# Optimization experiments

Hardware: AMD Instinct MI355X
Metric: run time of the kernel (lower is better)

Reference implementation:

```python
import jax, jax.numpy as jnp
import numpy as np

DIM = 2048
N_HEADS = 16
HEAD_DIM = DIM // N_HEADS
MAX_SEQ_LEN = 2048
THRESHOLD = 0.7
LN_EPS = 1e-5


def _layernorm(x, g, b):
    mu = jnp.mean(x, axis=-1, keepdims=True)
    var = jnp.mean(jnp.square(x - mu), axis=-1, keepdims=True)
    return (x - mu) * jax.lax.rsqrt(var + LN_EPS) * g + b


def _act_quant(x):
    # 8-bit absmax activation quantization (per-tensor), straight-through
    s = 127.0 / jnp.maximum(jnp.max(jnp.abs(x)), 1e-5)
    xq = jnp.clip(jnp.round(x * s), -128.0, 127.0) / s
    return x + jax.lax.stop_gradient(xq - x)


def _ternary_quant(w):
    # W1.58 ternary: zero weights below threshold*mean|w|, scale = mean |w| over survivors
    delta = THRESHOLD * jnp.mean(jnp.abs(w))
    mask = (jnp.abs(w) > delta).astype(w.dtype)
    alpha = jnp.sum(jnp.abs(w) * mask) / jnp.maximum(jnp.sum(mask), 1.0)
    wq = jnp.sign(w) * mask * alpha
    return w + jax.lax.stop_gradient(wq - w)


def _bitlinear(x, w, g, b):
    x = _layernorm(x, g, b)
    xq = _act_quant(x)
    wq = _ternary_quant(w)
    return xq @ wq.T


def _rope_tables():
    inv = 1.0 / (10000.0 ** (np.arange(0, HEAD_DIM, 2, dtype=np.float32) / HEAD_DIM))
    t = np.arange(MAX_SEQ_LEN, dtype=np.float32)
    ang = np.outer(t, inv)  # (max_seq, head_dim/2)
    return jnp.asarray(np.cos(ang)), jnp.asarray(np.sin(ang))


def _apply_rope(x, cos_t, sin_t):
    # Faithful to source: x is (B, H, S, D) and freqs are indexed by x.shape[1] == H
    n = x.shape[1]
    xr = x.reshape(*x.shape[:-1], HEAD_DIM // 2, 2)
    a, b = xr[..., 0], xr[..., 1]
    c = cos_t[:n][None, :, None, :]  # (1, H, 1, D/2)
    s = sin_t[:n][None, :, None, :]
    out = jnp.stack([a * c - b * s, a * s + b * c], axis=-1)
    return out.reshape(x.shape)


def setup_inputs() -> dict:
    key = jax.random.key(0)
    ks = jax.random.split(key, 5)
    std = np.sqrt(2.0 / DIM)
    d = {"x": jax.random.normal(ks[0], (2, MAX_SEQ_LEN, DIM), dtype=jnp.float32)}
    for i, nm in enumerate(["q", "k", "v", "o"]):
        d[f"w_{nm}"] = jax.random.normal(ks[i + 1], (DIM, DIM), dtype=jnp.float32) * std
        d[f"g_{nm}"] = jnp.ones((DIM,), dtype=jnp.float32)
        d[f"b_{nm}"] = jnp.zeros((DIM,), dtype=jnp.float32)
    return d


def reference(x, w_q, g_q, b_q, w_k, g_k, b_k, w_v, g_v, b_v, w_o, g_o, b_o):
    B, S, _ = x.shape
    cos_t, sin_t = _rope_tables()
    scale = HEAD_DIM ** -0.5

    def split_heads(t):
        return t.reshape(B, S, N_HEADS, HEAD_DIM).transpose(0, 2, 1, 3)

    q = split_heads(_bitlinear(x, w_q, g_q, b_q))
    k = split_heads(_bitlinear(x, w_k, g_k, b_k))
    v = split_heads(_bitlinear(x, w_v, g_v, b_v))
    q = _apply_rope(q, cos_t, sin_t)
    k = _apply_rope(k, cos_t, sin_t)
    scores = jnp.einsum("bhsd,bhtd->bhst", q, k) * scale
    attn = jax.nn.softmax(scores, axis=-1)
    out = jnp.einsum("bhst,bhtd->bhsd", attn, v)
    out = out.transpose(0, 2, 1, 3).reshape(B, S, DIM)
    return _bitlinear(out, w_o, g_o, b_o)
```

## Files before the change

### kernel.cpp

```cpp
#include <hip/hip_runtime.h>
#include <math.h>

#define DIM 2048
#define NROWS 4096
#define WN (DIM*DIM)
#define HEADS 16
#define HDIM 128
#define SEQ 2048

typedef __attribute__((ext_vector_type(8))) short short8;
typedef __attribute__((ext_vector_type(8))) _Float16 half8;
typedef __attribute__((ext_vector_type(4))) float floatx4;
typedef __attribute__((ext_vector_type(4))) int intx4;

__device__ __forceinline__ unsigned short f2h(float f) {
  _Float16 h = (_Float16)f;
  return __builtin_bit_cast(unsigned short, h);
}
__device__ __forceinline__ float h2f(unsigned short u) {
  _Float16 h = __builtin_bit_cast(_Float16, u);
  return (float)h;
}
__device__ __forceinline__ unsigned pkh2(float a, float b) {
  return __builtin_bit_cast(unsigned, __builtin_amdgcn_cvt_pkrtz(a, b));
}

__device__ __forceinline__ void gload_lds16(const void* g, void* l) {
  __builtin_amdgcn_global_load_lds(
      (const __attribute__((address_space(1))) unsigned int*)g,
      (__attribute__((address_space(3))) unsigned int*)l, 16, 0, 0);
}

__device__ __forceinline__ float wredSum(float v) {
  #pragma unroll
  for (int o = 1; o < 64; o <<= 1) v += __shfl_xor(v, o);
  return v;
}
__device__ __forceinline__ float wredMax(float v) {
  #pragma unroll
  for (int o = 1; o < 64; o <<= 1) v = fmaxf(v, __shfl_xor(v, o));
  return v;
}

__device__ __forceinline__ float blockReduceSum(float v, float* red) {
  int tid = threadIdx.x;
  red[tid] = v; __syncthreads();
  for (int s = 128; s > 0; s >>= 1) {
    if (tid < s) red[tid] += red[tid + s];
    __syncthreads();
  }
  float r = red[0]; __syncthreads();
  return r;
}

__device__ __forceinline__ const float* pick_w(const float* a, const float* b,
                                               const float* c, const float* d, int i) {
  return i == 0 ? a : i == 1 ? b : i == 2 ? c : d;
}

__global__ __launch_bounds__(256) void w_abs_partial(
    const float* w0, const float* w1, const float* w2, const float* w3, float* part)
{
  const float4* w4 = (const float4*)pick_w(w0, w1, w2, w3, blockIdx.y);
  float s = 0.f;
  for (int i = blockIdx.x * 256 + threadIdx.x; i < WN / 4; i += 1024 * 256) {
    float4 v = w4[i];
    s += fabsf(v.x) + fabsf(v.y) + fabsf(v.z) + fabsf(v.w);
  }
  __shared__ float red[256];
  float t = blockReduceSum(s, red);
  if (threadIdx.x == 0) part[blockIdx.y * 1024 + blockIdx.x] = t;
}

__global__ __launch_bounds__(256) void w_delta_final(const float* part, float* stats)
{
  float s = 0.f;
  for (int i = threadIdx.x; i < 1024; i += 256) s += part[blockIdx.x * 1024 + i];
  __shared__ float red[256];
  float t = blockReduceSum(s, red);
  if (threadIdx.x == 0) stats[blockIdx.x] = 0.7f * (t / (float)WN);
}

__device__ __forceinline__ signed char tq(float v, float delta) {
  if (fabsf(v) > delta) return (v > 0.f) ? (signed char)1 : (signed char)-1;
  return (signed char)0;
}

__global__ __launch_bounds__(256) void w_maskquant(
    const float* w0, const float* w1, const float* w2, const float* w3,
    const float* stats, float* part2, signed char* tern)
{
  int wi = blockIdx.y;
  const float4* w4 = (const float4*)pick_w(w0, w1, w2, w3, wi);
  float delta = stats[wi];
  char4* out = (char4*)(tern + (size_t)wi * WN);
  float s = 0.f, cnt = 0.f;
  for (int i = blockIdx.x * 256 + threadIdx.x; i < WN / 4; i += 1024 * 256) {
    float4 v = w4[i];
    char4 o;
    float a;
    a = fabsf(v.x); if (a > delta) { s += a; cnt += 1.f; } o.x = tq(v.x, delta);
    a = fabsf(v.y); if (a > delta) { s += a; cnt += 1.f; } o.y = tq(v.y, delta);
    a = fabsf(v.z); if (a > delta) { s += a; cnt += 1.f; } o.z = tq(v.z, delta);
    a = fabsf(v.w); if (a > delta) { s += a; cnt += 1.f; } o.w = tq(v.w, delta);
    out[i] = o;
  }
  __shared__ float red[256];
  float ts = blockReduceSum(s, red);
  float tc = blockReduceSum(cnt, red);
  if (threadIdx.x == 0) {
    part2[((size_t)blockIdx.y * 1024 + blockIdx.x) * 2]     = ts;
    part2[((size_t)blockIdx.y * 1024 + blockIdx.x) * 2 + 1] = tc;
  }
}

__global__ __launch_bounds__(256) void w_alpha_final(const float* part2, float* stats)
{
  float s = 0.f, c = 0.f;
  for (int i = threadIdx.x; i < 1024; i += 256) {
    s += part2[((size_t)blockIdx.x * 1024 + i) * 2];
    c += part2[((size_t)blockIdx.x * 1024 + i) * 2 + 1];
  }
  __shared__ float red[256];
  float ts = blockReduceSum(s, red);
  float tc = blockReduceSum(c, red);
  if (threadIdx.x == 0) stats[4 + blockIdx.x] = ts / fmaxf(tc, 1.f);
}

__global__ __launch_bounds__(256) void ln_absmax3(
    const float* __restrict__ x,
    const float* __restrict__ g0, const float* __restrict__ b0,
    const float* __restrict__ g1, const float* __restrict__ b1,
    const float* __restrict__ g2, const float* __restrict__ b2,
    float* __restrict__ pmax)
{
  const int lane = threadIdx.x & 63;
  const int row = blockIdx.x * 4 + (threadIdx.x >> 6);
  const float* xr = x + (size_t)row * DIM;
  float4 a[8];
  float s = 0.f, sq = 0.f;
  #pragma unroll
  for (int j = 0; j < 8; ++j) {
    a[j] = *(const float4*)(xr + j * 256 + lane * 4);
    s  += a[j].x + a[j].y + a[j].z + a[j].w;
    sq += a[j].x*a[j].x + a[j].y*a[j].y + a[j].z*a[j].z + a[j].w*a[j].w;
  }
  s = wredSum(s); sq = wredSum(sq);
  float mu = s * (1.f / DIM);
  float var = sq * (1.f / DIM) - mu * mu;
  float rstd = 1.f / sqrtf(var + 1e-5f);
  const float* gs[3] = {g0, g1, g2};
  const float* bs[3] = {b0, b1, b2};
  #pragma unroll
  for (int p = 0; p < 3; ++p) {
    float m = 0.f;
    #pragma unroll
    for (int j = 0; j < 8; ++j) {
      float4 gg = *(const float4*)(gs[p] + j * 256 + lane * 4);
      float4 bb = *(const float4*)(bs[p] + j * 256 + lane * 4);
      m = fmaxf(m, fabsf((a[j].x - mu) * rstd * gg.x + bb.x));
      m = fmaxf(m, fabsf((a[j].y - mu) * rstd * gg.y + bb.y));
      m = fmaxf(m, fabsf((a[j].z - mu) * rstd * gg.z + bb.z));
      m = fmaxf(m, fabsf((a[j].w - mu) * rstd * gg.w + bb.w));
    }
    m = wredMax(m);
    if (lane == 0) pmax[(size_t)p * NROWS + row] = m;
  }
}

__global__ __launch_bounds__(256) void absmax_final(
    const float* __restrict__ pmax, unsigned* __restrict__ ambits)
{
  const float* src = pmax + (size_t)blockIdx.x * NROWS;
  float m = 0.f;
  for (int i = threadIdx.x; i < NROWS; i += 256) m = fmaxf(m, src[i]);
  m = wredMax(m);
  __shared__ float red[4];
  if ((threadIdx.x & 63) == 0) red[threadIdx.x >> 6] = m;
  __syncthreads();
  if (threadIdx.x == 0)
    ambits[blockIdx.x] = __float_as_uint(fmaxf(fmaxf(red[0], red[1]), fmaxf(red[2], red[3])));
}

__global__ __launch_bounds__(256) void ln_quant3(
    const float* __restrict__ x,
    const float* __restrict__ g0, const float* __restrict__ b0,
    const float* __restrict__ g1, const float* __restrict__ b1,
    const float* __restrict__ g2, const float* __restrict__ b2,
    const unsigned* __restrict__ ambits,
    signed char* __restrict__ xq0, signed char* __restrict__ xq1,
    signed char* __restrict__ xq2)
{
  const int lane = threadIdx.x & 63;
  const int row = blockIdx.x * 4 + (threadIdx.x >> 6);
  const float* xr = x + (size_t)row * DIM;
  float4 a[8];
  float s = 0.f, sq = 0.f;
  #pragma unroll
  for (int j = 0; j < 8; ++j) {
    a[j] = *(const float4*)(xr + j * 256 + lane * 4);
    s  += a[j].x + a[j].y + a[j].z + a[j].w;
    sq += a[j].x*a[j].x + a[j].y*a[j].y + a[j].z*a[j].z + a[j].w*a[j].w;
  }
  s = wredSum(s); sq = wredSum(sq);
  float mu = s * (1.f / DIM);
  float var = sq * (1.f / DIM) - mu * mu;
  float rstd = 1.f / sqrtf(var + 1e-5f);
  const float* gs[3] = {g0, g1, g2};
  const float* bs[3] = {b0, b1, b2};
  signed char* outs[3] = {xq0, xq1, xq2};
  #pragma unroll
  for (int p = 0; p < 3; ++p) {
    float sc = 127.f / fmaxf(__uint_as_float(ambits[p]), 1e-5f);
    #pragma unroll
    for (int j = 0; j < 8; ++j) {
      float4 gg = *(const float4*)(gs[p] + j * 256 + lane * 4);
      float4 bb = *(const float4*)(bs[p] + j * 256 + lane * 4);
      float y0 = (a[j].x - mu) * rstd * gg.x + bb.x;
      float y1 = (a[j].y - mu) * rstd * gg.y + bb.y;
      float y2 = (a[j].z - mu) * rstd * gg.z + bb.z;
      float y3 = (a[j].w - mu) * rstd * gg.w + bb.w;
      char4 q;
      q.x = (signed char)(int)fminf(fmaxf(rintf(y0 * sc), -128.f), 127.f);
      q.y = (signed char)(int)fminf(fmaxf(rintf(y1 * sc), -128.f), 127.f);
      q.z = (signed char)(int)fminf(fmaxf(rintf(y2 * sc), -128.f), 127.f);
      q.w = (signed char)(int)fminf(fmaxf(rintf(y3 * sc), -128.f), 127.f);
      *(char4*)(outs[p] + (size_t)row * DIM + j * 256 + lane * 4) = q;
    }
  }
}

template<int MODE>
__global__ __launch_bounds__(256) void ln_kernel(
    const float* __restrict__ x, const float* __restrict__ g, const float* __restrict__ bias,
    const unsigned* __restrict__ ambits, float* __restrict__ pmax,
    signed char* __restrict__ xq)
{
  const int lane = threadIdx.x & 63;
  const int row = blockIdx.x * 4 + (threadIdx.x >> 6);
  const float* xr = x + (size_t)row * DIM;
  float4 a[8];
  float s = 0.f, sq = 0.f;
  #pragma unroll
  for (int j = 0; j < 8; ++j) {
    a[j] = *(const float4*)(xr + j * 256 + lane * 4);
    s  += a[j].x + a[j].y + a[j].z + a[j].w;
    sq += a[j].x*a[j].x + a[j].y*a[j].y + a[j].z*a[j].z + a[j].w*a[j].w;
  }
  s = wredSum(s); sq = wredSum(sq);
  float mu = s * (1.f / DIM);
  float var = sq * (1.f / DIM) - mu * mu;
  float rstd = 1.f / sqrtf(var + 1e-5f);
  if (MODE == 0) {
    float m = 0.f;
    #pragma unroll
    for (int j = 0; j < 8; ++j) {
      float4 gg = *(const float4*)(g + j * 256 + lane * 4);
      float4 bb = *(const float4*)(bias + j * 256 + lane * 4);
      m = fmaxf(m, fabsf((a[j].x - mu) * rstd * gg.x + bb.x));
      m = fmaxf(m, fabsf((a[j].y - mu) * rstd * gg.y + bb.y));
      m = fmaxf(m, fabsf((a[j].z - mu) * rstd * gg.z + bb.z));
      m = fmaxf(m, fabsf((a[j].w - mu) * rstd * gg.w + bb.w));
    }
    m = wredMax(m);
    if (lane == 0) pmax[row] = m;
  } else {
    float sc = 127.f / fmaxf(__uint_as_float(*ambits), 1e-5f);
    #pragma unroll
    for (int j = 0; j < 8; ++j) {
      float4 gg = *(const float4*)(g + j * 256 + lane * 4);
      float4 bb = *(const float4*)(bias + j * 256 + lane * 4);
      float y0 = (a[j].x - mu) * rstd * gg.x + bb.x;
      float y1 = (a[j].y - mu) * rstd * gg.y + bb.y;
      float y2 = (a[j].z - mu) * rstd * gg.z + bb.z;
      float y3 = (a[j].w - mu) * rstd * gg.w + bb.w;
      char4 q;
      q.x = (signed char)(int)fminf(fmaxf(rintf(y0 * sc), -128.f), 127.f);
      q.y = (signed char)(int)fminf(fmaxf(rintf(y1 * sc), -128.f), 127.f);
      q.z = (signed char)(int)fminf(fmaxf(rintf(y2 * sc), -128.f), 127.f);
      q.w = (signed char)(int)fminf(fmaxf(rintf(y3 * sc), -128.f), 127.f);
      *(char4*)(xq + (size_t)row * DIM + j * 256 + lane * 4) = q;
    }
  }
}

__global__ __launch_bounds__(256) void gemm_qkv(
    const signed char* __restrict__ A0, const signed char* __restrict__ A1,
    const signed char* __restrict__ A2, const signed char* __restrict__ Bt0,
    unsigned short* __restrict__ C0, unsigned short* __restrict__ C1,
    unsigned short* __restrict__ C2t, const float* __restrict__ stats)
{
  const int tid = threadIdx.x;
  const int lane = tid & 63;
  const int w = tid >> 6;
  const int wm = w >> 1, wn = w & 1;
  const int quad = lane >> 4, l16 = lane & 15;
  const int bm = blockIdx.x * 128, bn = blockIdx.y * 128;
  const int z = blockIdx.z;

  const signed char* A  = z == 0 ? A0 : z == 1 ? A1 : A2;
  const signed char* Bt = Bt0 + (size_t)z * WN;

  __shared__ __align__(16) signed char smem[2 * 128 * 128];
  signed char* As = smem;
  signed char* Bs = smem + 128 * 128;

  const int srow_off = lane >> 3;
  const int scol     = (lane & 7) * 16;

  intx4 acc[4][4];
  #pragma unroll
  for (int i = 0; i < 4; ++i)
    #pragma unroll
    for (int j = 0; j < 4; ++j) acc[i][j] = {0, 0, 0, 0};

  for (int k0 = 0; k0 < DIM; k0 += 128) {
    #pragma unroll
    for (int i = 0; i < 4; ++i) {
      int c = i * 4 + w;
      int row = c * 8 + srow_off;
      gload_lds16(A  + (size_t)(bm + row) * DIM + k0 + scol, &As[c * 1024]);
      gload_lds16(Bt + (size_t)(bn + row) * DIM + k0 + scol, &Bs[c * 1024]);
    }
    __syncthreads();
    #pragma unroll
    for (int kc = 0; kc < 2; ++kc) {
      intx4 af[4], bf[4];
      #pragma unroll
      for (int i = 0; i < 4; ++i)
        af[i] = *(const intx4*)&As[(wm * 64 + i * 16 + l16) * 128 + kc * 64 + quad * 16];
      #pragma unroll
      for (int j = 0; j < 4; ++j)
        bf[j] = *(const intx4*)&Bs[(wn * 64 + j * 16 + l16) * 128 + kc * 64 + quad * 16];
      #pragma unroll
      for (int i = 0; i < 4; ++i)
        #pragma unroll
        for (int j = 0; j < 4; ++j)
          acc[i][j] = __builtin_amdgcn_mfma_i32_16x16x64_i8(af[i], bf[j], acc[i][j], 0, 0, 0);
    }
    __syncthreads();
  }

  const unsigned* am = (const unsigned*)(stats + 8);
  float scale = stats[4 + z] * fmaxf(__uint_as_float(am[z]), 1e-5f) * (1.f / 127.f);

  if (z < 2) {
    unsigned short* Cp = z == 0 ? C0 : C1;
    #pragma unroll
    for (int i = 0; i < 4; ++i)
      #pragma unroll
      for (int j = 0; j < 4; ++j)
        #pragma unroll
        for (int r = 0; r < 4; ++r) {
          int m = bm + wm * 64 + i * 16 + quad * 4 + r;
          int n = bn + wn * 64 + j * 16 + l16;
          Cp[(size_t)m * DIM + n] = f2h((float)acc[i][j][r] * scale);
        }
  } else {
    #pragma unroll
    for (int i = 0; i < 4; ++i)
      #pragma unroll
      for (int j = 0; j < 4; ++j)
        #pragma unroll
        for (int r = 0; r < 4; ++r) {
          int s = wm * 64 + i * 16 + quad * 4 + r;
          int d = wn * 64 + j * 16 + l16;
          int byte = (d * 256 + s * 2) ^ ((d & 7) << 4);
          *(unsigned short*)(smem + byte) = f2h((float)acc[i][j][r] * scale);
        }
    __syncthreads();
    const int b = bm >> 11;
    const int s_base = bm & (SEQ - 1);
    const int h = blockIdx.y;
    const int sc = (tid & 15) * 8;
    #pragma unroll
    for (int pass = 0; pass < 8; ++pass) {
      int d = (tid >> 4) + pass * 16;
      int byte = (d * 256 + sc * 2) ^ ((d & 7) << 4);
      *(uint4*)(C2t + ((size_t)(b * HEADS + h) * HDIM + d) * SEQ + s_base + sc) =
          *(const uint4*)(smem + byte);
    }
  }
}

__global__ __launch_bounds__(256) void gemm_bt(
    const signed char* __restrict__ A, const signed char* __restrict__ Bt,
    float* __restrict__ Cp, const float* __restrict__ stats, int wi)
{
  const int tid = threadIdx.x;
  const int lane = tid & 63;
  const int w = tid >> 6;
  const int wm = w >> 1, wn = w & 1;
  const int quad = lane >> 4, l16 = lane & 15;
  const int bm = blockIdx.x * 128, bn = blockIdx.y * 128;

  __shared__ __align__(16) signed char As[128 * 128];
  __shared__ __align__(16) signed char Bs[128 * 128];

  const int srow_off = lane >> 3;
  const int scol     = (lane & 7) * 16;

  intx4 acc[4][4];
  #pragma unroll
  for (int i = 0; i < 4; ++i)
    #pragma unroll
    for (int j = 0; j < 4; ++j) acc[i][j] = {0, 0, 0, 0};

  for (int k0 = 0; k0 < DIM; k0 += 128) {
    #pragma unroll
    for (int i = 0; i < 4; ++i) {
      int c = i * 4 + w;
      int row = c * 8 + srow_off;
      gload_lds16(A  + (size_t)(bm + row) * DIM + k0 + scol, &As[c * 1024]);
      gload_lds16(Bt + (size_t)(bn + row) * DIM + k0 + scol, &Bs[c * 1024]);
    }
    __syncthreads();
    #pragma unroll
    for (int kc = 0; kc < 2; ++kc) {
      intx4 af[4], bf[4];
      #pragma unroll
      for (int i = 0; i < 4; ++i)
        af[i] = *(const intx4*)&As[(wm * 64 + i * 16 + l16) * 128 + kc * 64 + quad * 16];
      #pragma unroll
      for (int j = 0; j < 4; ++j)
        bf[j] = *(const intx4*)&Bs[(wn * 64 + j * 16 + l16) * 128 + kc * 64 + quad * 16];
      #pragma unroll
      for (int i = 0; i < 4; ++i)
        #pragma unroll
        for (int j = 0; j < 4; ++j)
          acc[i][j] = __builtin_amdgcn_mfma_i32_16x16x64_i8(af[i], bf[j], acc[i][j], 0, 0, 0);
    }
    __syncthreads();
  }

  const unsigned* am = (const unsigned*)(stats + 8);
  float scale = stats[4 + wi] * fmaxf(__uint_as_float(am[wi]), 1e-5f) * (1.f / 127.f);
  #pragma unroll
  for (int i = 0; i < 4; ++i)
    #pragma unroll
    for (int j = 0; j < 4; ++j)
      #pragma unroll
      for (int r = 0; r < 4; ++r) {
        int m = bm + wm * 64 + i * 16 + quad * 4 + r;
        int n = bn + wn * 64 + j * 16 + l16;
        Cp[(size_t)m * DIM + n] = (float)acc[i][j][r] * scale;
      }
}

__global__ __launch_bounds__(256) void rope_kernel(unsigned short* q, unsigned short* k)
{
  const float SC = 0.12751741769011063f;
  int idx = blockIdx.x * 256 + threadIdx.x;
  int p = idx & 63;
  int h = (idx >> 6) & (HEADS - 1);
  int r = idx >> 10;
  float inv = exp2f((float)p * -0.20762050593046f);
  float ang = (float)h * inv;
  float sn, cs;
  __sincosf(ang, &sn, &cs);
  size_t base = (size_t)r * DIM + h * HDIM + 2 * p;
  {
    float a = h2f(q[base]), b = h2f(q[base + 1]);
    q[base]     = f2h((a * cs - b * sn) * SC);
    q[base + 1] = f2h((a * sn + b * cs) * SC);
  }
  {
    float a = h2f(k[base]), b = h2f(k[base + 1]);
    k[base]     = f2h(a * cs - b * sn);
    k[base + 1] = f2h(a * sn + b * cs);
  }
}

__global__ __launch_bounds__(256, 2) void flash_attn(
    const unsigned short* __restrict__ qf, const unsigned short* __restrict__ kf,
    const unsigned short* __restrict__ vt, float* __restrict__ o)
{
  const int tid = threadIdx.x;
  const int lane = tid & 63;
  const int w = tid >> 6;
  const int quad = lane >> 4;
  const int l16 = lane & 15;
  const int L = blockIdx.x;
  const int slot = L >> 3;
  const int bh = ((L & 7) << 2) | (slot >> 4);
  const int qt = slot & 15;
  const int b = bh >> 4;
  const int h = bh & 15;

  __shared__ __align__(16) char Ks[64 * 256];
  __shared__ __align__(16) char Vs[128 * 128];
  __shared__ __align__(16) char Ps[4][32 * 128];

  const size_t qbase = ((size_t)(b * SEQ + qt * 128 + w * 32 + l16)) * DIM + h * HDIM;
  short8 qa[2][4];
  #pragma unroll
  for (int f = 0; f < 2; ++f)
    #pragma unroll
    for (int kc = 0; kc < 4; ++kc)
      qa[f][kc] = *(const short8*)(qf + qbase + (size_t)f * 16 * DIM + kc * 32 + quad * 8);

  float m_q[2] = {-INFINITY, -INFINITY};
  float l_q[2] = {0.f, 0.f};
  floatx4 accO0[8], accO1[8];
  #pragma unroll
  for (int i = 0; i < 8; ++i) { accO0[i] = {0.f, 0.f, 0.f, 0.f}; accO1[i] = {0.f, 0.f, 0.f, 0.f}; }

  const char* kg = (const char*)(kf + (size_t)(b * SEQ) * DIM + h * HDIM);
  const char* vg = (const char*)(vt + (size_t)bh * HDIM * SEQ);

  int koff[4], voff[4];
  #pragma unroll
  for (int j = 0; j < 4; ++j) {
    int c = w * 4 + j;
    int rK = c * 4 + (lane >> 4);
    koff[j] = rK * (DIM * 2) + (((lane & 15) * 16) ^ ((rK & 7) << 4));
    int rV = c * 8 + (lane >> 3);
    voff[j] = rV * (SEQ * 2) + (((lane & 7) * 16) ^ ((rV & 7) << 4));
  }

  for (int kt = 0; kt < SEQ / 64; ++kt) {
    __syncthreads();
    const char* kgb = kg + (size_t)kt * 64 * DIM * 2;
    const char* vgb = vg + (size_t)kt * 128;
    #pragma unroll
    for (int j = 0; j < 4; ++j) {
      int c = w * 4 + j;
      gload_lds16(kgb + koff[j], &Ks[c * 1024]);
      gload_lds16(vgb + voff[j], &Vs[c * 1024]);
    }
    asm volatile("s_waitcnt vmcnt(0)" ::: "memory");
    __syncthreads();

    float sreg[2][4][4];
    __builtin_amdgcn_s_setprio(1);
    #pragma unroll
    for (int jt = 0; jt < 4; ++jt) {
      floatx4 a0 = {0.f, 0.f, 0.f, 0.f}, a1 = {0.f, 0.f, 0.f, 0.f};
      #pragma unroll
      for (int kc = 0; kc < 4; ++kc) {
        int kr = jt * 16 + l16;
        short8 kb = *(const short8*)&Ks[(kr * 256 + kc * 64 + quad * 16) ^ ((kr & 7) << 4)];
        a0 = __builtin_amdgcn_mfma_f32_16x16x32_f16(
            __builtin_bit_cast(half8, kb), __builtin_bit_cast(half8, qa[0][kc]), a0, 0, 0, 0);
        a1 = __builtin_amdgcn_mfma_f32_16x16x32_f16(
            __builtin_bit_cast(half8, kb), __builtin_bit_cast(half8, qa[1][kc]), a1, 0, 0, 0);
      }
      #pragma unroll
      for (int r = 0; r < 4; ++r) { sreg[0][jt][r] = a0[r]; sreg[1][jt][r] = a1[r]; }
    }
    __builtin_amdgcn_s_setprio(0);

    float alpha[2]; int need[2];
    #pragma unroll
    for (int f = 0; f < 2; ++f) {
      float mx = sreg[f][0][0];
      #pragma unroll
      for (int jt = 0; jt < 4; ++jt)
        #pragma unroll
        for (int r = 0; r < 4; ++r) mx = fmaxf(mx, sreg[f][jt][r]);
      mx = fmaxf(mx, __shfl_xor(mx, 16));
      mx = fmaxf(mx, __shfl_xor(mx, 32));
      need[f] = !__all(mx <= m_q[f] + 8.f);
      float mnew;
      if (need[f]) {
        mnew = fmaxf(m_q[f], mx);
        alpha[f] = exp2f(m_q[f] - mnew);
        m_q[f] = mnew;
      } else {
        mnew = m_q[f];
        alpha[f] = 1.f;
      }
      float ssum = 0.f;
      #pragma unroll
      for (int jt = 0; jt < 4; ++jt) {
        float p0 = exp2f(sreg[f][jt][0] - mnew);
        float p1 = exp2f(sreg[f][jt][1] - mnew);
        float p2 = exp2f(sreg[f][jt][2] - mnew);
        float p3 = exp2f(sreg[f][jt][3] - mnew);
        uint2 pk2;
        pk2.x = pkh2(p0, p1);
        pk2.y = pkh2(p2, p3);
        ssum += (p0 + p1) + (p2 + p3);
        *(uint2*)&Ps[w][((f * 16 + l16) * 128 + jt * 32 + quad * 8) ^ ((l16 & 7) << 4)] = pk2;
      }
      ssum += __shfl_xor(ssum, 16);
      ssum += __shfl_xor(ssum, 32);
      l_q[f] = l_q[f] * alpha[f] + ssum;
    }
    if (need[0]) {
      #pragma unroll
      for (int dt = 0; dt < 8; ++dt)
        #pragma unroll
        for (int r = 0; r < 4; ++r) accO0[dt][r] *= alpha[0];
    }
    if (need[1]) {
      #pragma unroll
      for (int dt = 0; dt < 8; ++dt)
        #pragma unroll
        for (int r = 0; r < 4; ++r) accO1[dt][r] *= alpha[1];
    }

    __builtin_amdgcn_s_setprio(1);
    #pragma unroll
    for (int kc = 0; kc < 2; ++kc) {
      short8 pf0 = *(const short8*)&Ps[w][(l16 * 128 + kc * 64 + quad * 16) ^ ((l16 & 7) << 4)];
      short8 pf1 = *(const short8*)&Ps[w][((16 + l16) * 128 + kc * 64 + quad * 16) ^ ((l16 & 7) << 4)];
      #pragma unroll
      for (int dt = 0; dt < 8; ++dt) {
        int vr = dt * 16 + l16;
        short8 vf = *(const short8*)&Vs[(vr * 128 + kc * 64 + quad * 16) ^ ((vr & 7) << 4)];
        accO0[dt] = __builtin_amdgcn_mfma_f32_16x16x32_f16(
            __builtin_bit_cast(half8, vf), __builtin_bit_cast(half8, pf0), accO0[dt], 0, 0, 0);
        accO1[dt] = __builtin_amdgcn_mfma_f32_16x16x32_f16(
            __builtin_bit_cast(half8, vf), __builtin_bit_cast(half8, pf1), accO1[dt], 0, 0, 0);
      }
    }
    __builtin_amdgcn_s_setprio(0);
  }

  #pragma unroll
  for (int f = 0; f < 2; ++f) {
    float invl = 1.0f / l_q[f];
    const size_t obase = (size_t)(b * SEQ + qt * 128 + w * 32 + f * 16 + l16) * DIM + h * HDIM;
    #pragma unroll
    for (int dt = 0; dt < 8; ++dt) {
      floatx4 acc = f == 0 ? accO0[dt] : accO1[dt];
      float4 ov;
      ov.x = acc[0] * invl; ov.y = acc[1] * invl;
      ov.z = acc[2] * invl; ov.w = acc[3] * invl;
      *(float4*)(o + obase + dt * 16 + quad * 4) = ov;
    }
  }
}

extern "C" void kernel_launch(void* const* d_in, const int* in_sizes, int n_in,
                              void* d_out, int out_size, void* d_ws, size_t ws_size,
                              hipStream_t stream)
{
  (void)in_sizes; (void)n_in; (void)out_size; (void)ws_size;
  const float* x = (const float*)d_in[0];
  const float* w[4]; const float* g[4]; const float* bb[4];
  for (int i = 0; i < 4; ++i) {
    w[i]  = (const float*)d_in[1 + 3 * i];
    g[i]  = (const float*)d_in[2 + 3 * i];
    bb[i] = (const float*)d_in[3 + 3 * i];
  }

  char* base = (char*)d_ws;
  size_t off = 0;
  auto alloc = [&](size_t bytes) {
    char* p = base + off;
    off += (bytes + 255) & ~(size_t)255;
    return p;
  };
  const size_t ACTH = (size_t)NROWS * DIM * 2;
  const size_t ACT8 = (size_t)NROWS * DIM;
  float* stats          = (float*)alloc(64);
  float* part1          = (float*)alloc(4 * 1024 * sizeof(float));
  float* part2          = (float*)alloc(4 * 1024 * 2 * sizeof(float));
  float* pmax           = (float*)alloc((size_t)4 * NROWS * sizeof(float));
  signed char* tern     = (signed char*)alloc((size_t)4 * WN);
  signed char* xq0      = (signed char*)alloc(ACT8);
  signed char* xq1      = (signed char*)alloc(ACT8);
  signed char* xq2      = (signed char*)alloc(ACT8);
  unsigned short* qh    = (unsigned short*)alloc(ACTH);
  unsigned short* kh    = (unsigned short*)alloc(ACTH);
  unsigned short* vtb   = (unsigned short*)alloc(ACTH);
  float* oat            = (float*)alloc((size_t)NROWS * DIM * sizeof(float));
  signed char* xqo = xq0;
  unsigned* ambits = (unsigned*)(stats + 8);

  hipMemsetAsync(stats, 0, 64, stream);

  dim3 b256(256);
  w_abs_partial<<<dim3(1024, 4), b256, 0, stream>>>(w[0], w[1], w[2], w[3], part1);
  w_delta_final<<<4, b256, 0, stream>>>(part1, stats);
  w_maskquant<<<dim3(1024, 4), b256, 0, stream>>>(w[0], w[1], w[2], w[3], stats, part2, tern);
  w_alpha_final<<<4, b256, 0, stream>>>(part2, stats);

  ln_absmax3<<<NROWS / 4, b256, 0, stream>>>(x, g[0], bb[0], g[1], bb[1], g[2], bb[2], pmax);
  absmax_final<<<3, b256, 0, stream>>>(pmax, ambits);
  ln_quant3<<<NROWS / 4, b256, 0, stream>>>(x, g[0], bb[0], g[1], bb[1], g[2], bb[2], ambits,
                                            xq0, xq1, xq2);

  gemm_qkv<<<dim3(NROWS / 128, DIM / 128, 3), b256, 0, stream>>>(
      xq0, xq1, xq2, tern, qh, kh, vtb, stats);

  rope_kernel<<<NROWS * 1024 / 256, b256, 0, stream>>>(qh, kh);
  flash_attn<<<dim3(16 * 32), b256, 0, stream>>>(qh, kh, vtb, oat);

  ln_kernel<0><<<NROWS / 4, b256, 0, stream>>>(oat, g[3], bb[3], nullptr,
                                               pmax + (size_t)3 * NROWS, nullptr);
  absmax_final<<<1, b256, 0, stream>>>(pmax + (size_t)3 * NROWS, ambits + 3);
  ln_kernel<1><<<NROWS / 4, b256, 0, stream>>>(oat, g[3], bb[3], ambits + 3, nullptr, xqo);
  gemm_bt<<<dim3(NROWS / 128, DIM / 128), b256, 0, stream>>>(
      xqo, tern + (size_t)3 * WN, (float*)d_out, stats, 3);
}
```

Before: 429.8 us.

## Split attention KV range in two, fuse RoPE into QKV GEMM epilogue

Flash attention now splits each (batch, head, q-tile) across two blocks covering halves of the key sequence. Each block writes fp16 partial outputs plus a log-sum-exp value, and the output-projection layernorm kernels merge the two halves. The grid doubles to 1024 blocks and occupancy is raised to 3 blocks per SM to fill more CUs. The separate RoPE kernel is removed and rotation is applied in the QKV GEMM epilogue through a lane shuffle. The float attention output buffer is replaced with two fp16 buffers, which adds partial-merge work and some precision loss.

Result: slower. 583.9 us (+35.9%).

```diff
diff --git a/kernel.cpp b/kernel.cpp
--- a/kernel.cpp
+++ b/kernel.cpp
@@ -232,18 +232,31 @@
 
 template<int MODE>
 __global__ __launch_bounds__(256) void ln_kernel(
-    const float* __restrict__ x, const float* __restrict__ g, const float* __restrict__ bias,
+    const unsigned short* __restrict__ po0, const unsigned short* __restrict__ po1,
+    const float* __restrict__ lm,
+    const float* __restrict__ g, const float* __restrict__ bias,
     const unsigned* __restrict__ ambits, float* __restrict__ pmax,
     signed char* __restrict__ xq)
 {
   const int lane = threadIdx.x & 63;
   const int row = blockIdx.x * 4 + (threadIdx.x >> 6);
-  const float* xr = x + (size_t)row * DIM;
   float4 a[8];
   float s = 0.f, sq = 0.f;
   #pragma unroll
   for (int j = 0; j < 8; ++j) {
-    a[j] = *(const float4*)(xr + j * 256 + lane * 4);
+    int h_e = j * 2 + (lane >> 5);
+    float L1 = lm[(size_t)row * HEADS + h_e];
+    float L2 = lm[(size_t)NROWS * HEADS + (size_t)row * HEADS + h_e];
+    float Lm = fmaxf(L1, L2);
+    float wa = exp2f(L1 - Lm), wb = exp2f(L2 - Lm);
+    float rs = 1.f / (wa + wb);
+    wa *= rs; wb *= rs;
+    ushort4 u1 = *(const ushort4*)(po0 + (size_t)row * DIM + j * 256 + lane * 4);
+    ushort4 u2 = *(const ushort4*)(po1 + (size_t)row * DIM + j * 256 + lane * 4);
+    a[j].x = wa * h2f(u1.x) + wb * h2f(u2.x);
+    a[j].y = wa * h2f(u1.y) + wb * h2f(u2.y);
+    a[j].z = wa * h2f(u1.z) + wb * h2f(u2.z);
+    a[j].w = wa * h2f(u1.w) + wb * h2f(u2.w);
     s  += a[j].x + a[j].y + a[j].z + a[j].w;
     sq += a[j].x*a[j].x + a[j].y*a[j].y + a[j].z*a[j].z + a[j].w*a[j].w;
   }
@@ -345,6 +358,20 @@
   float scale = stats[4 + z] * fmaxf(__uint_as_float(am[z]), 1e-5f) * (1.f / 127.f);
 
   if (z < 2) {
+    const float SC = 0.12751741769011063f;
+    const int hh = blockIdx.y;
+    const int odd = l16 & 1;
+    float cs[4], sn[4];
+    #pragma unroll
+    for (int j = 0; j < 4; ++j) {
+      int p = (wn * 64 + j * 16 + l16) >> 1;
+      float inv = exp2f((float)p * -0.20762050593046f);
+      float ang = (float)hh * inv;
+      float ss, cc;
+      __sincosf(ang, &ss, &cc);
+      if (z == 0) { ss *= SC; cc *= SC; }
+      cs[j] = cc; sn[j] = ss;
+    }
     unsigned short* Cp = z == 0 ? C0 : C1;
     #pragma unroll
     for (int i = 0; i < 4; ++i)
@@ -354,7 +381,10 @@
         for (int r = 0; r < 4; ++r) {
           int m = bm + wm * 64 + i * 16 + quad * 4 + r;
           int n = bn + wn * 64 + j * 16 + l16;
-          Cp[(size_t)m * DIM + n] = f2h((float)acc[i][j][r] * scale);
+          float v = (float)acc[i][j][r] * scale;
+          float pv = __shfl_xor(v, 1);
+          float out = odd ? (pv * sn[j] + v * cs[j]) : (v * cs[j] - pv * sn[j]);
+          Cp[(size_t)m * DIM + n] = f2h(out);
         }
   } else {
     #pragma unroll
@@ -447,33 +477,11 @@
       }
 }
 
-__global__ __launch_bounds__(256) void rope_kernel(unsigned short* q, unsigned short* k)
-{
-  const float SC = 0.12751741769011063f;
-  int idx = blockIdx.x * 256 + threadIdx.x;
-  int p = idx & 63;
-  int h = (idx >> 6) & (HEADS - 1);
-  int r = idx >> 10;
-  float inv = exp2f((float)p * -0.20762050593046f);
-  float ang = (float)h * inv;
-  float sn, cs;
-  __sincosf(ang, &sn, &cs);
-  size_t base = (size_t)r * DIM + h * HDIM + 2 * p;
-  {
-    float a = h2f(q[base]), b = h2f(q[base + 1]);
-    q[base]     = f2h((a * cs - b * sn) * SC);
-    q[base + 1] = f2h((a * sn + b * cs) * SC);
-  }
-  {
-    float a = h2f(k[base]), b = h2f(k[base + 1]);
-    k[base]     = f2h(a * cs - b * sn);
-    k[base + 1] = f2h(a * sn + b * cs);
-  }
-}
-
-__global__ __launch_bounds__(256, 2) void flash_attn(
+__global__ __launch_bounds__(256, 3) void flash_attn(
     const unsigned short* __restrict__ qf, const unsigned short* __restrict__ kf,
-    const unsigned short* __restrict__ vt, float* __restrict__ o)
+    const unsigned short* __restrict__ vt,
+    unsigned short* __restrict__ po0, unsigned short* __restrict__ po1,
+    float* __restrict__ lm)
 {
   const int tid = threadIdx.x;
   const int lane = tid & 63;
@@ -482,8 +490,10 @@
   const int l16 = lane & 15;
   const int L = blockIdx.x;
   const int slot = L >> 3;
-  const int bh = ((L & 7) << 2) | (slot >> 4);
-  const int qt = slot & 15;
+  const int bh = ((L & 7) << 2) | (slot >> 5);
+  const int rem = slot & 31;
+  const int qt = rem >> 1;
+  const int half = rem & 1;
   const int b = bh >> 4;
   const int h = bh & 15;
 
@@ -518,7 +528,7 @@
     voff[j] = rV * (SEQ * 2) + (((lane & 7) * 16) ^ ((rV & 7) << 4));
   }
 
-  for (int kt = 0; kt < SEQ / 64; ++kt) {
+  for (int kt = half * 16; kt < half * 16 + 16; ++kt) {
     __syncthreads();
     const char* kgb = kg + (size_t)kt * 64 * DIM * 2;
     const char* vgb = vg + (size_t)kt * 128;
@@ -618,17 +628,21 @@
     __builtin_amdgcn_s_setprio(0);
   }
 
+  unsigned short* po = half ? po1 : po0;
   #pragma unroll
   for (int f = 0; f < 2; ++f) {
     float invl = 1.0f / l_q[f];
-    const size_t obase = (size_t)(b * SEQ + qt * 128 + w * 32 + f * 16 + l16) * DIM + h * HDIM;
+    const size_t qrow = (size_t)(b * SEQ + qt * 128 + w * 32 + f * 16 + l16);
+    if (quad == 0)
+      lm[(size_t)half * NROWS * HEADS + qrow * HEADS + h] = m_q[f] + log2f(l_q[f]);
+    const size_t obase = qrow * DIM + h * HDIM;
     #pragma unroll
     for (int dt = 0; dt < 8; ++dt) {
       floatx4 acc = f == 0 ? accO0[dt] : accO1[dt];
-      float4 ov;
-      ov.x = acc[0] * invl; ov.y = acc[1] * invl;
-      ov.z = acc[2] * invl; ov.w = acc[3] * invl;
-      *(float4*)(o + obase + dt * 16 + quad * 4) = ov;
+      ushort4 ov;
+      ov.x = f2h(acc[0] * invl); ov.y = f2h(acc[1] * invl);
+      ov.z = f2h(acc[2] * invl); ov.w = f2h(acc[3] * invl);
+      *(ushort4*)(po + obase + dt * 16 + quad * 4) = ov;
     }
   }
 }
@@ -659,6 +673,7 @@
   float* part1          = (float*)alloc(4 * 1024 * sizeof(float));
   float* part2          = (float*)alloc(4 * 1024 * 2 * sizeof(float));
   float* pmax           = (float*)alloc((size_t)4 * NROWS * sizeof(float));
+  float* lm             = (float*)alloc((size_t)2 * NROWS * HEADS * sizeof(float));
   signed char* tern     = (signed char*)alloc((size_t)4 * WN);
   signed char* xq0      = (signed char*)alloc(ACT8);
   signed char* xq1      = (signed char*)alloc(ACT8);
@@ -666,7 +681,8 @@
   unsigned short* qh    = (unsigned short*)alloc(ACTH);
   unsigned short* kh    = (unsigned short*)alloc(ACTH);
   unsigned short* vtb   = (unsigned short*)alloc(ACTH);
-  float* oat            = (float*)alloc((size_t)NROWS * DIM * sizeof(float));
+  unsigned short* po0   = (unsigned short*)alloc(ACTH);
+  unsigned short* po1   = (unsigned short*)alloc(ACTH);
   signed char* xqo = xq0;
   unsigned* ambits = (unsigned*)(stats + 8);
 
@@ -686,13 +702,13 @@
   gemm_qkv<<<dim3(NROWS / 128, DIM / 128, 3), b256, 0, stream>>>(
       xq0, xq1, xq2, tern, qh, kh, vtb, stats);
 
-  rope_kernel<<<NROWS * 1024 / 256, b256, 0, stream>>>(qh, kh);
-  flash_attn<<<dim3(16 * 32), b256, 0, stream>>>(qh, kh, vtb, oat);
-
-  ln_kernel<0><<<NROWS / 4, b256, 0, stream>>>(oat, g[3], bb[3], nullptr,
+  flash_attn<<<dim3(32 * 32), b256, 0, stream>>>(qh, kh, vtb, po0, po1, lm);
+
+  ln_kernel<0><<<NROWS / 4, b256, 0, stream>>>(po0, po1, lm, g[3], bb[3], nullptr,
                                                pmax + (size_t)3 * NROWS, nullptr);
   absmax_final<<<1, b256, 0, stream>>>(pmax + (size_t)3 * NROWS, ambits + 3);
-  ln_kernel<1><<<NROWS / 4, b256, 0, stream>>>(oat, g[3], bb[3], ambits + 3, nullptr, xqo);
+  ln_kernel<1><<<NROWS / 4, b256, 0, stream>>>(po0, po1, lm, g[3], bb[3], ambits + 3,
+                                               nullptr, xqo);
   gemm_bt<<<dim3(NROWS / 128, DIM / 128), b256, 0, stream>>>(
       xqo, tern + (size_t)3 * WN, (float*)d_out, stats, 3);
 }
```
